# Kernel tuning notes

Hardware: AMD Instinct MI355X
Metric: run time of the kernel (lower is better)

## Reference

```python
import jax, jax.numpy as jnp
import numpy as np
import math

B, SV, ST, D, H = 16, 1024, 512, 768, 8
DH = D // H


def layernorm(x, g, b, eps=1e-5):
    m = jnp.mean(x, axis=-1, keepdims=True)
    v = jnp.var(x, axis=-1, keepdims=True)
    return (x - m) / jnp.sqrt(v + eps) * g + b


def setup_inputs() -> dict:
    key = jax.random.key(0)
    ks = jax.random.split(key, 12)
    s = 1.0 / math.sqrt(D)
    inp = {
        "visual_features": jax.random.normal(ks[0], (B, SV, D), jnp.float32),
        "text_features": jax.random.normal(ks[1], (B, ST, D), jnp.float32),
        "visual_mask": jnp.ones((B, SV), jnp.int32),
        "text_mask": jnp.ones((B, ST), jnp.int32),
        "Wq": jax.random.normal(ks[2], (D, D), jnp.float32) * s,
        "bq": jnp.zeros((D,), jnp.float32),
        "Wk": jax.random.normal(ks[3], (D, D), jnp.float32) * s,
        "bk": jnp.zeros((D,), jnp.float32),
        "Wv": jax.random.normal(ks[4], (D, D), jnp.float32) * s,
        "bv": jnp.zeros((D,), jnp.float32),
        "Wo": jax.random.normal(ks[5], (D, D), jnp.float32) * s,
        "bo": jnp.zeros((D,), jnp.float32),
        "ln1_g": jnp.ones((D,), jnp.float32),
        "ln1_b": jnp.zeros((D,), jnp.float32),
        "Wf": jax.random.normal(ks[6], (2 * D, D), jnp.float32) * (1.0 / math.sqrt(2 * D)),
        "bf": jnp.zeros((D,), jnp.float32),
        "ln2_g": jnp.ones((D,), jnp.float32),
        "ln2_b": jnp.zeros((D,), jnp.float32),
    }
    return inp


def _heads(x):
    b, s, _ = x.shape
    return x.reshape(b, s, H, DH)


def _cross_attn(q_feats, kv_feats, kv_mask, Wq, bq, Wk, bk, Wv, bv):
    # q_feats: [B,Sq,D], kv_feats: [B,Sk,D], kv_mask: [B,Sk] or None
    q = _heads(q_feats @ Wq + bq)   # [B,Sq,H,DH]
    k = _heads(kv_feats @ Wk + bk)  # [B,Sk,H,DH]
    v = _heads(kv_feats @ Wv + bv)
    scores = jnp.einsum('bqhd,bkhd->bhqk', q, k) / math.sqrt(DH)
    if kv_mask is not None:
        scores = jnp.where(kv_mask[:, None, None, :] == 0, -jnp.inf, scores)
    attn = jax.nn.softmax(scores, axis=-1)  # dropout is identity in eval
    out = jnp.einsum('bhqk,bkhd->bqhd', attn, v)
    return out.reshape(q_feats.shape[0], q_feats.shape[1], D)


def reference(visual_features, text_features, visual_mask, text_mask,
              Wq, bq, Wk, bk, Wv, bv, Wo, bo, ln1_g, ln1_b,
              Wf, bf, ln2_g, ln2_b):
    # visual queries attend to text
    v2t = _cross_attn(visual_features, text_features, text_mask, Wq, bq, Wk, bk, Wv, bv)
    # text queries attend to visual
    t2v = _cross_attn(text_features, visual_features, visual_mask, Wq, bq, Wk, bk, Wv, bv)
    attended_visual = layernorm(visual_features + (v2t @ Wo + bo), ln1_g, ln1_b)
    attended_text = layernorm(text_features + (t2v @ Wo + bo), ln1_g, ln1_b)
    # masked mean pooling
    vm = visual_mask[:, :, None].astype(jnp.float32)
    pooled_v = (attended_visual * vm).sum(1) / vm.sum(1)
    tm = text_mask[:, :, None].astype(jnp.float32)
    pooled_t = (attended_text * tm).sum(1) / tm.sum(1)
    fused = jnp.concatenate([pooled_v, pooled_t], axis=-1) @ Wf + bf
    fused = layernorm(fused, ln2_g, ln2_b)  # dropout identity in eval
    return fused
```

## Files before the change

kernel.cpp:

```cpp
#include <hip/hip_runtime.h>

typedef __bf16 bf16x8 __attribute__((ext_vector_type(8)));
typedef float f32x4 __attribute__((ext_vector_type(4)));
typedef unsigned short u16;
typedef unsigned int u32;
typedef u16 u16x8 __attribute__((ext_vector_type(8)));
typedef u16 u16x4 __attribute__((ext_vector_type(4)));


__device__ __forceinline__ u16 f2bf(float f) {
    u32 u = __builtin_bit_cast(u32, f);
    u32 r = u + 0x7FFFu + ((u >> 16) & 1u);
    return (u16)(r >> 16);
}

__device__ __forceinline__ float bf2f(u16 b) {
    u32 u = ((u32)b) << 16;
    return __builtin_bit_cast(float, u);
}

__device__ __forceinline__ f32x4 mfma16(bf16x8 a, bf16x8 b, f32x4 c) {
    return __builtin_amdgcn_mfma_f32_16x16x32_bf16(a, b, c, 0, 0, 0);
}

#define GLOAD_LDS16(g, l) __builtin_amdgcn_global_load_lds( \
    (__attribute__((address_space(1))) void*)(g), \
    (__attribute__((address_space(3))) void*)(l), 16, 0, 0)


__global__ __launch_bounds__(256) void k_cvt_x(const float* __restrict__ vf,
                                               const float* __restrict__ tf,
                                               u16* __restrict__ X, int nvis4) {
    int i = blockIdx.x * 256 + threadIdx.x;
    f32x4 v = (i < nvis4) ? ((const f32x4*)vf)[i] : ((const f32x4*)tf)[i - nvis4];
    u16x4 o = { f2bf(v[0]), f2bf(v[1]), f2bf(v[2]), f2bf(v[3]) };
    ((u16x4*)X)[i] = o;
}

__global__ __launch_bounds__(256) void k_transpose(const float* __restrict__ src,
                                                   u16* __restrict__ dst,
                                                   int K0, int N0) {
    __shared__ float t[64][65];
    int ntx = N0 >> 6;
    int k0 = (blockIdx.x / ntx) << 6, n0 = (blockIdx.x % ntx) << 6;
    int c = threadIdx.x & 63, rr = threadIdx.x >> 6;
#pragma unroll
    for (int q = 0; q < 16; q++) {
        int r = q * 4 + rr;
        t[r][c] = src[(size_t)(k0 + r) * N0 + n0 + c];
    }
    __syncthreads();
#pragma unroll
    for (int q = 0; q < 16; q++) {
        int r = q * 4 + rr;
        dst[(size_t)(n0 + r) * K0 + k0 + c] = f2bf(t[c][r]);
    }
}

__global__ __launch_bounds__(256) void k_bias(const float* __restrict__ bq,
                                              const float* __restrict__ bk,
                                              const float* __restrict__ bv,
                                              float* __restrict__ bqkv) {
    int n = blockIdx.x * 256 + threadIdx.x;
    if (n < 2304) {
        const float* s = (n < 768) ? bq : ((n < 1536) ? bk : bv);
        int r = (n < 768) ? n : ((n < 1536) ? n - 768 : n - 1536);
        bqkv[n] = s[r];
    }
}

__global__ __launch_bounds__(256) void k_zero(float* __restrict__ p) {
    p[blockIdx.x * 256 + threadIdx.x] = 0.f;
}

template <bool OUT_BF16, bool ADD_RES, bool SPLIT_VT>
__global__ __launch_bounds__(256) void k_gemm(const u16* __restrict__ A,
                                              const u16* __restrict__ Bt,
                                              const float* __restrict__ bias,
                                              const float* __restrict__ resA,
                                              const float* __restrict__ resB,
                                              void* __restrict__ Cout,
                                              int Ndim, int Kdim, int mvisL,
                                              u16* __restrict__ VtGp, int Rtot) {
    __shared__ alignas(16) u16 sA[2][128 * 32];
    __shared__ alignas(16) u16 sB[2][128 * 32];
    const int tid = threadIdx.x, wid = tid >> 6, lane = tid & 63;
    const int nwg = gridDim.x;
    const int wg = (blockIdx.x & 7) * (nwg >> 3) + (blockIdx.x >> 3);
    const int ntiles = Ndim >> 7;
    const int mt = wg / ntiles, nt = wg - mt * ntiles;
    const int m0 = mt << 7, n0 = nt << 7;
    const int wm = wid >> 1, wn = wid & 1;
    f32x4 acc[4][4] = {};

    const int r0 = tid >> 2, p0 = tid & 3;
    const int r1 = 64 + r0;
    const u16* ga0 = A + (size_t)(m0 + r0) * Kdim + p0 * 8;
    const u16* ga1 = A + (size_t)(m0 + r1) * Kdim + p0 * 8;
    const u16* gb0 = Bt + (size_t)(n0 + r0) * Kdim + p0 * 8;
    const u16* gb1 = Bt + (size_t)(n0 + r1) * Kdim + p0 * 8;
    const int loff0 = wid * 512;
    const int loff1 = 2048 + wid * 512;

    const int arow = (wm << 6) + (lane & 15);
    const int brow = (wn << 6) + (lane & 15);
    const int kg = (lane >> 4) * 8;

    auto stage = [&](int kt, int pb) {
        GLOAD_LDS16(ga0 + kt, &sA[pb][loff0]);
        GLOAD_LDS16(ga1 + kt, &sA[pb][loff1]);
        GLOAD_LDS16(gb0 + kt, &sB[pb][loff0]);
        GLOAD_LDS16(gb1 + kt, &sB[pb][loff1]);
    };

    const int niter = Kdim >> 5;
    stage(0, 0);
    for (int it = 0; it < niter; ++it) {
        const int cur = it & 1;
        __syncthreads();
        if (it + 1 < niter) stage((it + 1) << 5, cur ^ 1);
        bf16x8 av[4], bw[4];
#pragma unroll
        for (int i = 0; i < 4; i++) av[i] = *(const bf16x8*)&sA[cur][(arow + i * 16) * 32 + kg];
#pragma unroll
        for (int j = 0; j < 4; j++) bw[j] = *(const bf16x8*)&sB[cur][(brow + j * 16) * 32 + kg];
#pragma unroll
        for (int i = 0; i < 4; i++)
#pragma unroll
            for (int j = 0; j < 4; j++) acc[i][j] = mfma16(av[i], bw[j], acc[i][j]);
    }

    const int col0 = n0 + (wn << 6) + (lane & 15);
    const int rowb = m0 + (wm << 6) + ((lane >> 4) << 2);
    float bvals[4];
#pragma unroll
    for (int j = 0; j < 4; j++) bvals[j] = bias[col0 + j * 16];

    if constexpr (SPLIT_VT) {
        if (n0 >= 1536) {
            const int vcol0 = col0 - 1536;
#pragma unroll
            for (int i = 0; i < 4; i++) {
#pragma unroll
                for (int j = 0; j < 4; j++) {
                    u16x4 o4;
#pragma unroll
                    for (int rg = 0; rg < 4; rg++) o4[rg] = f2bf(acc[i][j][rg] + bvals[j]);
                    *(u16x4*)&VtGp[(size_t)(vcol0 + j * 16) * Rtot + rowb + i * 16] = o4;
                }
            }
            return;
        }
    }

#pragma unroll
    for (int i = 0; i < 4; i++) {
#pragma unroll
        for (int rg = 0; rg < 4; rg++) {
            const int row = rowb + i * 16 + rg;
            const float* rp = nullptr;
            if constexpr (ADD_RES)
                rp = (row < mvisL) ? resA + (size_t)row * 768
                                   : resB + (size_t)(row - mvisL) * 768;
#pragma unroll
            for (int j = 0; j < 4; j++) {
                const int col = col0 + j * 16;
                float v = acc[i][j][rg] + bvals[j];
                if constexpr (ADD_RES) v += rp[col];
                if constexpr (OUT_BF16)
                    ((u16*)Cout)[(size_t)row * Ndim + col] = f2bf(v);
                else
                    ((float*)Cout)[(size_t)row * Ndim + col] = v;
            }
        }
    }
}

__global__ __launch_bounds__(512) void k_attn(const u16* __restrict__ qkv,
                                              const u16* __restrict__ VtG,
                                              const int* __restrict__ vmaskc,
                                              const int* __restrict__ tmaskc,
                                              u16* __restrict__ attn, int CHn, int Rtot) {
    __shared__ alignas(16) u16 Kl[2][128 * 128];
    __shared__ alignas(16) u16 Vt[2][96 * 128];
    __shared__ alignas(16) u16 Pl[8][16 * 128];
    __shared__ float mk[2][128];

    const int bx = blockIdx.x;
    int b, h, qbase, kbase, nqt, ntl;
    const int* mask;
    const int vcap = CHn * 8;
    if (bx < vcap) {
        b = bx >> 3; h = bx & 7;
        qbase = b << 10; kbase = (CHn << 10) + (b << 9);
        mask = tmaskc + (b << 9); nqt = 4; ntl = 2;
    } else {
        const int bx2 = bx - vcap;
        b = bx2 >> 3; h = bx2 & 7;
        qbase = (CHn << 10) + (b << 9); kbase = b << 10;
        mask = vmaskc + (b << 10); nqt = 2; ntl = 3;
    }
    const int ntile = 1 << ntl;
    const int nsteps = nqt << ntl;
    const int tid = threadIdx.x, wid = tid >> 6, lane = tid & 63;
    const int l15 = lane & 15, l4 = lane >> 4;
    const float scale = 0.10206207261596577f;

    int koff[4];
#pragma unroll
    for (int kk = 0; kk < 4; kk++) koff[kk] = ((kk * 4 + l4) ^ (l15 & 7)) << 3;

    auto kt_of = [&](int s) {
        const int qt = s >> ntl, ktr = s & (ntile - 1);
        return (qt & 1) ? (ntile - 1 - ktr) : ktr;
    };
    auto stage = [&](int kt, int pb) {
#pragma unroll
        for (int it = 0; it < 4; ++it) {
            const int cb = it * 512 + (wid << 6);
            const int c = cb + lane;
            const int r = c >> 4, s8 = c & 15;
            const int k8 = s8 ^ (r & 7);
            const u16* src = qkv + (size_t)(kbase + (kt << 7) + r) * 2304 + 768 + h * 96
                             + (k8 < 12 ? k8 * 8 : 0);
            GLOAD_LDS16(src, &Kl[pb][(size_t)cb * 8]);
        }
#pragma unroll
        for (int it = 0; it < 3; ++it) {
            const int cb = it * 512 + (wid << 6);
            const int c = cb + lane;
            const int d = c >> 4, s8 = c & 15;
            const int k8 = s8 ^ (d & 7);
            const u16* src = VtG + (size_t)(h * 96 + d) * Rtot + kbase + (kt << 7) + k8 * 8;
            GLOAD_LDS16(src, &Vt[pb][(size_t)cb * 8]);
        }
        if (tid < 128) mk[pb][tid] = mask[(kt << 7) + tid] ? 0.f : -1e30f;
    };

    stage(kt_of(0), 0);
    int s = 0;
    for (int qt = 0; qt < nqt; ++qt) {
        bf16x8 aq[2][3];
#pragma unroll
        for (int qs = 0; qs < 2; ++qs) {
            const int qr = qbase + (qt << 8) + (wid << 5) + qs * 16 + l15;
#pragma unroll
            for (int kk = 0; kk < 3; kk++) {
                bf16x8 tq = *(const bf16x8*)&qkv[(size_t)qr * 2304 + h * 96 + kk * 32 + l4 * 8];
#pragma unroll
                for (int e = 0; e < 8; e++) tq[e] = (__bf16)((float)tq[e] * scale);
                aq[qs][kk] = tq;
            }
        }
        f32x4 o[2][6] = {};
        float mrun[2][4], lrun[2][4];
#pragma unroll
        for (int qs = 0; qs < 2; ++qs)
#pragma unroll
            for (int rg = 0; rg < 4; rg++) { mrun[qs][rg] = -1e30f; lrun[qs][rg] = 0.f; }

        for (int ktr = 0; ktr < ntile; ++ktr, ++s) {
            const int cur = s & 1;
            __syncthreads();
            if (s + 1 < nsteps) stage(kt_of(s + 1), cur ^ 1);

            f32x4 sc[2][8];
#pragma unroll
            for (int j = 0; j < 8; j++) {
                const int rbase = (j * 16 + l15) * 128;
                bf16x8 bk[3];
#pragma unroll
                for (int kk = 0; kk < 3; kk++)
                    bk[kk] = *(const bf16x8*)&Kl[cur][rbase + koff[kk]];
#pragma unroll
                for (int qs = 0; qs < 2; ++qs) {
                    f32x4 cj = {0.f, 0.f, 0.f, 0.f};
#pragma unroll
                    for (int kk = 0; kk < 3; kk++) cj = mfma16(aq[qs][kk], bk[kk], cj);
                    sc[qs][j] = cj;
                }
            }

#pragma unroll
            for (int qs = 0; qs < 2; ++qs) {
                float tmax[4] = {-1e30f, -1e30f, -1e30f, -1e30f};
#pragma unroll
                for (int j = 0; j < 8; j++) {
                    float mb = mk[cur][j * 16 + l15];
#pragma unroll
                    for (int rg = 0; rg < 4; rg++) {
                        float v = sc[qs][j][rg] + mb;
                        sc[qs][j][rg] = v;
                        tmax[rg] = fmaxf(tmax[rg], v);
                    }
                }
#pragma unroll
                for (int d = 1; d < 16; d <<= 1)
#pragma unroll
                    for (int rg = 0; rg < 4; rg++)
                        tmax[rg] = fmaxf(tmax[rg], __shfl_xor(tmax[rg], d));
                int need = 0;
#pragma unroll
                for (int rg = 0; rg < 4; rg++) need |= (tmax[rg] > mrun[qs][rg] + 8.f) ? 1 : 0;
                if (__any(need)) {
#pragma unroll
                    for (int rg = 0; rg < 4; rg++) {
                        float mn = fmaxf(mrun[qs][rg], tmax[rg]);
                        float corr = __expf(mrun[qs][rg] - mn);
                        mrun[qs][rg] = mn;
                        lrun[qs][rg] *= corr;
#pragma unroll
                        for (int j6 = 0; j6 < 6; j6++) o[qs][j6][rg] *= corr;
                    }
                }
                float tsum[4] = {0.f, 0.f, 0.f, 0.f};
#pragma unroll
                for (int j = 0; j < 8; j++)
#pragma unroll
                    for (int rg = 0; rg < 4; rg++) {
                        float p = __expf(sc[qs][j][rg] - mrun[qs][rg]);
                        tsum[rg] += p;
                        const int prow = l4 * 4 + rg;
                        Pl[wid][prow * 128 + ((j * 16 + l15) ^ ((prow & 7) << 3))] = f2bf(p);
                    }
#pragma unroll
                for (int d = 1; d < 16; d <<= 1)
#pragma unroll
                    for (int rg = 0; rg < 4; rg++) tsum[rg] += __shfl_xor(tsum[rg], d);
#pragma unroll
                for (int rg = 0; rg < 4; rg++) lrun[qs][rg] += tsum[rg];

#pragma unroll
                for (int kk = 0; kk < 4; kk++) {
                    bf16x8 ap = *(const bf16x8*)&Pl[wid][l15 * 128 + koff[kk]];
#pragma unroll
                    for (int j6 = 0; j6 < 6; j6++) {
                        bf16x8 bv8 = *(const bf16x8*)&Vt[cur][(j6 * 16 + l15) * 128 + koff[kk]];
                        o[qs][j6] = mfma16(ap, bv8, o[qs][j6]);
                    }
                }
            }
        }

#pragma unroll
        for (int qs = 0; qs < 2; ++qs) {
            float inv[4];
#pragma unroll
            for (int rg = 0; rg < 4; rg++) inv[rg] = 1.f / lrun[qs][rg];
            const size_t orow = (size_t)(qbase + (qt << 8) + (wid << 5) + qs * 16);
#pragma unroll
            for (int j6 = 0; j6 < 6; j6++)
#pragma unroll
                for (int rg = 0; rg < 4; rg++)
                    attn[(orow + l4 * 4 + rg) * 768 + h * 96 + j6 * 16 + l15] =
                        f2bf(o[qs][j6][rg] * inv[rg]);
        }
    }
}

__global__ __launch_bounds__(256) void k_ln_pool(const u16* __restrict__ X,
                                                 const int* __restrict__ vmaskc,
                                                 const int* __restrict__ tmaskc,
                                                 const float* __restrict__ g,
                                                 const float* __restrict__ bb,
                                                 float* __restrict__ pooled,
                                                 int mvisL, int bg0) {
    __shared__ float pool[768];
    const int tid = threadIdx.x, wid = tid >> 6, lane = tid & 63;
    const int row0 = blockIdx.x << 5;
    const bool vis = row0 < mvisL;
    const int* mask = vis ? vmaskc : tmaskc;
    const int mbase = vis ? 0 : mvisL;
    const int bl = vis ? (row0 >> 10) : ((row0 - mvisL) >> 9);
    float* pout = pooled + (vis ? 0 : 12288) + (size_t)(bg0 + bl) * 768;

    float gv[12], bv2[12];
#pragma unroll
    for (int k = 0; k < 12; k++) { gv[k] = g[lane + k * 64]; bv2[k] = bb[lane + k * 64]; }
    float acc[12] = {};
    for (int rr = 0; rr < 8; ++rr) {
        const int row = row0 + (wid << 3) + rr;
        const u16* x = X + (size_t)row * 768;
        float xs[12], sm = 0.f, s2 = 0.f;
#pragma unroll
        for (int k = 0; k < 12; k++) {
            float tv = bf2f(x[lane + k * 64]);
            xs[k] = tv; sm += tv; s2 += tv * tv;
        }
#pragma unroll
        for (int d = 1; d < 64; d <<= 1) { sm += __shfl_xor(sm, d); s2 += __shfl_xor(s2, d); }
        const float mean = sm * (1.f / 768.f);
        const float rstd = rsqrtf(s2 * (1.f / 768.f) - mean * mean + 1e-5f);
        const float mv = (float)mask[row - mbase];
#pragma unroll
        for (int k = 0; k < 12; k++) acc[k] += ((xs[k] - mean) * rstd * gv[k] + bv2[k]) * mv;
    }
    pool[tid] = 0.f; pool[tid + 256] = 0.f; pool[tid + 512] = 0.f;
    __syncthreads();
#pragma unroll
    for (int k = 0; k < 12; k++) atomicAdd(&pool[lane + k * 64], acc[k]);
    __syncthreads();
    atomicAdd(&pout[tid], pool[tid]);
    atomicAdd(&pout[tid + 256], pool[tid + 256]);
    atomicAdd(&pout[tid + 512], pool[tid + 512]);
}

__device__ __forceinline__ float blk_sum(float v, volatile float* tmp) {
#pragma unroll
    for (int d = 1; d < 64; d <<= 1) v += __shfl_xor(v, d);
    __syncthreads();
    if ((threadIdx.x & 63) == 0) tmp[threadIdx.x >> 6] = v;
    __syncthreads();
    return tmp[0] + tmp[1] + tmp[2] + tmp[3];
}

__global__ __launch_bounds__(256) void k_final(const float* __restrict__ pooled,
                                               const int* __restrict__ vmask,
                                               const int* __restrict__ tmask,
                                               const float* __restrict__ Wf,
                                               const float* __restrict__ bfv,
                                               const float* __restrict__ g2,
                                               const float* __restrict__ b2,
                                               float* __restrict__ out) {
    __shared__ float sh[1536];
    __shared__ float red[4];
    const int b = blockIdx.x, tid = threadIdx.x;
    float cv = 0.f, ct = 0.f;
    for (int i = tid; i < 1024; i += 256) cv += (float)vmask[(b << 10) + i];
    for (int i = tid; i < 512; i += 256) ct += (float)tmask[(b << 9) + i];
    cv = blk_sum(cv, red);
    ct = blk_sum(ct, red);
    const float iv = 1.f / cv, itv = 1.f / ct;
#pragma unroll
    for (int k = 0; k < 3; k++) {
        int j = tid + (k << 8);
        sh[j] = pooled[b * 768 + j] * iv;
        sh[768 + j] = pooled[12288 + b * 768 + j] * itv;
    }
    __syncthreads();
    float f0 = bfv[tid], f1 = bfv[tid + 256], f2 = bfv[tid + 512];
    for (int i = 0; i < 1536; i++) {
        const float pv = sh[i];
        const float* w = Wf + (size_t)i * 768;
        f0 += pv * w[tid];
        f1 += pv * w[tid + 256];
        f2 += pv * w[tid + 512];
    }
    float sm = blk_sum(f0 + f1 + f2, red);
    float s2 = blk_sum(f0 * f0 + f1 * f1 + f2 * f2, red);
    const float mean = sm * (1.f / 768.f);
    const float rstd = rsqrtf(s2 * (1.f / 768.f) - mean * mean + 1e-5f);
    out[b * 768 + tid] = (f0 - mean) * rstd * g2[tid] + b2[tid];
    out[b * 768 + tid + 256] = (f1 - mean) * rstd * g2[tid + 256] + b2[tid + 256];
    out[b * 768 + tid + 512] = (f2 - mean) * rstd * g2[tid + 512] + b2[tid + 512];
}

extern "C" void kernel_launch(void* const* d_in, const int* in_sizes, int n_in,
                              void* d_out, int out_size, void* d_ws, size_t ws_size,
                              hipStream_t stream) {
    (void)in_sizes; (void)n_in; (void)out_size;
    const float* vf = (const float*)d_in[0];
    const float* tf = (const float*)d_in[1];
    const int* vmask = (const int*)d_in[2];
    const int* tmask = (const int*)d_in[3];
    const float* Wq = (const float*)d_in[4];
    const float* bq = (const float*)d_in[5];
    const float* Wk = (const float*)d_in[6];
    const float* bk = (const float*)d_in[7];
    const float* Wv = (const float*)d_in[8];
    const float* bv = (const float*)d_in[9];
    const float* Wo = (const float*)d_in[10];
    const float* bo = (const float*)d_in[11];
    const float* g1 = (const float*)d_in[12];
    const float* b1 = (const float*)d_in[13];
    const float* Wf = (const float*)d_in[14];
    const float* bfv = (const float*)d_in[15];
    const float* g2 = (const float*)d_in[16];
    const float* b2 = (const float*)d_in[17];
    float* outp = (float*)d_out;

    int CH = 16;
    while (CH > 1 && 4826112ull + (size_t)CH * 11796480ull > ws_size) CH >>= 1;
    const int NC = 16 / CH;
    const int Rtot = CH * 1536;

    char* ws = (char*)d_ws;
    u16*   wsW      = (u16*)(ws);
    u16*   wsWo     = (u16*)(ws + 3538944);
    float* wsBqkv   = (float*)(ws + 4718592);
    float* wsPooled = (float*)(ws + 4727808);
    u16*   wsX      = (u16*)(ws + 4826112);
    char*  qkvBase  = ws + 4826112 + (size_t)CH * 2359296;
    u16*   wsQKV    = (u16*)qkvBase;
    u16*   wsOproj  = (u16*)qkvBase;
    u16*   wsVtG    = (u16*)(qkvBase + (size_t)CH * 7077888);
    u16*   wsAttn   = wsX;

    k_transpose<<<dim3(144), dim3(256), 0, stream>>>(Wq, wsW, 768, 768);
    k_transpose<<<dim3(144), dim3(256), 0, stream>>>(Wk, wsW + 589824, 768, 768);
    k_transpose<<<dim3(144), dim3(256), 0, stream>>>(Wv, wsW + 1179648, 768, 768);
    k_transpose<<<dim3(144), dim3(256), 0, stream>>>(Wo, wsWo, 768, 768);
    k_bias<<<dim3(9), dim3(256), 0, stream>>>(bq, bk, bv, wsBqkv);
    k_zero<<<dim3(96), dim3(256), 0, stream>>>(wsPooled);

    for (int c = 0; c < NC; ++c) {
        const float* vfc = vf + (size_t)c * CH * 1024 * 768;
        const float* tfc = tf + (size_t)c * CH * 512 * 768;
        const int* vmc = vmask + c * CH * 1024;
        const int* tmc = tmask + c * CH * 512;

        k_cvt_x<<<dim3(CH * 1152), dim3(256), 0, stream>>>(vfc, tfc, wsX, CH * 196608);

        k_gemm<true, false, true><<<dim3(CH * 216), dim3(256), 0, stream>>>(
            wsX, wsW, wsBqkv, nullptr, nullptr, (void*)wsQKV, 2304, 768, 0, wsVtG, Rtot);

        k_attn<<<dim3(CH * 16), dim3(512), 0, stream>>>(
            wsQKV, wsVtG, vmc, tmc, wsAttn, CH, Rtot);

        k_gemm<true, true, false><<<dim3(CH * 72), dim3(256), 0, stream>>>(
            wsAttn, wsWo, bo, vfc, tfc, (void*)wsOproj, 768, 768, CH * 1024, nullptr, 0);

        k_ln_pool<<<dim3(CH * 48), dim3(256), 0, stream>>>(
            wsOproj, vmc, tmc, g1, b1, wsPooled, CH * 1024, c * CH);
    }

    k_final<<<dim3(16), dim3(256), 0, stream>>>(wsPooled, vmask, tmask, Wf, bfv, g2, b2, outp);
}
```

Measured before the change: 457.1 us.

## Keep softmax probabilities in registers via transposed QK^T and 16x16x16 PV MFMA

Swaps the operands of the QK^T MFMA so each lane holds scores for one query row across four key positions. That output layout then feeds directly as the A operand of a 16x16x16 bf16 MFMA for P·V, which removes the per-warp LDS round trip for P. Row max and sum reductions shrink from 4-step shuffles over 16 lanes to two cross-group shuffles with per-row scalars, and the correction factors are broadcast back with shuffles. In exchange it issues twice as many smaller-K MFMAs for P·V and reads V as 8-byte fragments.

Result: faster. 433.9 us (-5.1%).

```diff
diff --git a/kernel.cpp b/kernel.cpp
--- a/kernel.cpp
+++ b/kernel.cpp
@@ -1,6 +1,8 @@
 #include <hip/hip_runtime.h>
 
 typedef __bf16 bf16x8 __attribute__((ext_vector_type(8)));
+typedef __bf16 bf16x4v __attribute__((ext_vector_type(4)));
+typedef short s16x4 __attribute__((ext_vector_type(4)));
 typedef float f32x4 __attribute__((ext_vector_type(4)));
 typedef unsigned short u16;
 typedef unsigned int u32;
@@ -21,6 +23,20 @@
 
 __device__ __forceinline__ f32x4 mfma16(bf16x8 a, bf16x8 b, f32x4 c) {
     return __builtin_amdgcn_mfma_f32_16x16x32_bf16(a, b, c, 0, 0, 0);
+}
+
+__device__ __forceinline__ f32x4 mfma16k16(bf16x4v a, bf16x4v b, f32x4 c) {
+#if __has_builtin(__builtin_amdgcn_mfma_f32_16x16x16_bf16)
+    return __builtin_amdgcn_mfma_f32_16x16x16_bf16(a, b, c, 0, 0, 0);
+#elif __has_builtin(__builtin_amdgcn_mfma_f32_16x16x16bf16_1k)
+    return __builtin_amdgcn_mfma_f32_16x16x16bf16_1k(
+        __builtin_bit_cast(s16x4, a), __builtin_bit_cast(s16x4, b), c, 0, 0, 0);
+#else
+    f32x4 d;
+    asm volatile("v_mfma_f32_16x16x16_bf16 %0, %1, %2, %3"
+                 : "=v"(d) : "v"(a), "v"(b), "v"(c));
+    return d;
+#endif
 }
 
 #define GLOAD_LDS16(g, l) __builtin_amdgcn_global_load_lds( \
@@ -183,7 +199,6 @@
                                               u16* __restrict__ attn, int CHn, int Rtot) {
     __shared__ alignas(16) u16 Kl[2][128 * 128];
     __shared__ alignas(16) u16 Vt[2][96 * 128];
-    __shared__ alignas(16) u16 Pl[8][16 * 128];
     __shared__ float mk[2][128];
 
     const int bx = blockIdx.x;
@@ -206,9 +221,9 @@
     const int l15 = lane & 15, l4 = lane >> 4;
     const float scale = 0.10206207261596577f;
 
-    int koff[4];
-#pragma unroll
-    for (int kk = 0; kk < 4; kk++) koff[kk] = ((kk * 4 + l4) ^ (l15 & 7)) << 3;
+    int koff[3];
+#pragma unroll
+    for (int kk = 0; kk < 3; kk++) koff[kk] = ((kk * 4 + l4) ^ (l15 & 7)) << 3;
 
     auto kt_of = [&](int s) {
         const int qt = s >> ntl, ktr = s & (ntile - 1);
@@ -253,11 +268,8 @@
             }
         }
         f32x4 o[2][6] = {};
-        float mrun[2][4], lrun[2][4];
-#pragma unroll
-        for (int qs = 0; qs < 2; ++qs)
-#pragma unroll
-            for (int rg = 0; rg < 4; rg++) { mrun[qs][rg] = -1e30f; lrun[qs][rg] = 0.f; }
+        float mrunS[2] = {-1e30f, -1e30f};
+        float lrunS[2] = {0.f, 0.f};
 
         for (int ktr = 0; ktr < ntile; ++ktr, ++s) {
             const int cur = s & 1;
@@ -276,77 +288,79 @@
                 for (int qs = 0; qs < 2; ++qs) {
                     f32x4 cj = {0.f, 0.f, 0.f, 0.f};
 #pragma unroll
-                    for (int kk = 0; kk < 3; kk++) cj = mfma16(aq[qs][kk], bk[kk], cj);
+                    for (int kk = 0; kk < 3; kk++) cj = mfma16(bk[kk], aq[qs][kk], cj);
                     sc[qs][j] = cj;
                 }
             }
 
+            bf16x4v pb[2][8];
 #pragma unroll
             for (int qs = 0; qs < 2; ++qs) {
-                float tmax[4] = {-1e30f, -1e30f, -1e30f, -1e30f};
+                float tm = -1e30f;
 #pragma unroll
                 for (int j = 0; j < 8; j++) {
-                    float mb = mk[cur][j * 16 + l15];
+                    f32x4 m4 = *(const f32x4*)&mk[cur][j * 16 + (l4 << 2)];
 #pragma unroll
                     for (int rg = 0; rg < 4; rg++) {
-                        float v = sc[qs][j][rg] + mb;
+                        float v = sc[qs][j][rg] + m4[rg];
                         sc[qs][j][rg] = v;
-                        tmax[rg] = fmaxf(tmax[rg], v);
+                        tm = fmaxf(tm, v);
                     }
                 }
-#pragma unroll
-                for (int d = 1; d < 16; d <<= 1)
-#pragma unroll
-                    for (int rg = 0; rg < 4; rg++)
-                        tmax[rg] = fmaxf(tmax[rg], __shfl_xor(tmax[rg], d));
-                int need = 0;
-#pragma unroll
-                for (int rg = 0; rg < 4; rg++) need |= (tmax[rg] > mrun[qs][rg] + 8.f) ? 1 : 0;
+                tm = fmaxf(tm, __shfl_xor(tm, 16));
+                tm = fmaxf(tm, __shfl_xor(tm, 32));
+                const int need = (tm > mrunS[qs] + 8.f) ? 1 : 0;
                 if (__any(need)) {
+                    float mn = fmaxf(mrunS[qs], tm);
+                    float corrS = __expf(mrunS[qs] - mn);
+                    mrunS[qs] = mn;
+                    lrunS[qs] *= corrS;
+                    float cr[4];
+#pragma unroll
+                    for (int rg = 0; rg < 4; rg++) cr[rg] = __shfl(corrS, (l4 << 2) + rg);
+#pragma unroll
+                    for (int j6 = 0; j6 < 6; j6++)
+#pragma unroll
+                        for (int rg = 0; rg < 4; rg++) o[qs][j6][rg] *= cr[rg];
+                }
+                float ts = 0.f;
+#pragma unroll
+                for (int j = 0; j < 8; j++) {
+                    bf16x4v pq;
 #pragma unroll
                     for (int rg = 0; rg < 4; rg++) {
-                        float mn = fmaxf(mrun[qs][rg], tmax[rg]);
-                        float corr = __expf(mrun[qs][rg] - mn);
-                        mrun[qs][rg] = mn;
-                        lrun[qs][rg] *= corr;
-#pragma unroll
-                        for (int j6 = 0; j6 < 6; j6++) o[qs][j6][rg] *= corr;
+                        float p = __expf(sc[qs][j][rg] - mrunS[qs]);
+                        ts += p;
+                        pq[rg] = (__bf16)p;
                     }
+                    pb[qs][j] = pq;
                 }
-                float tsum[4] = {0.f, 0.f, 0.f, 0.f};
-#pragma unroll
-                for (int j = 0; j < 8; j++)
-#pragma unroll
-                    for (int rg = 0; rg < 4; rg++) {
-                        float p = __expf(sc[qs][j][rg] - mrun[qs][rg]);
-                        tsum[rg] += p;
-                        const int prow = l4 * 4 + rg;
-                        Pl[wid][prow * 128 + ((j * 16 + l15) ^ ((prow & 7) << 3))] = f2bf(p);
-                    }
-#pragma unroll
-                for (int d = 1; d < 16; d <<= 1)
-#pragma unroll
-                    for (int rg = 0; rg < 4; rg++) tsum[rg] += __shfl_xor(tsum[rg], d);
-#pragma unroll
-                for (int rg = 0; rg < 4; rg++) lrun[qs][rg] += tsum[rg];
-
-#pragma unroll
-                for (int kk = 0; kk < 4; kk++) {
-                    bf16x8 ap = *(const bf16x8*)&Pl[wid][l15 * 128 + koff[kk]];
-#pragma unroll
-                    for (int j6 = 0; j6 < 6; j6++) {
-                        bf16x8 bv8 = *(const bf16x8*)&Vt[cur][(j6 * 16 + l15) * 128 + koff[kk]];
-                        o[qs][j6] = mfma16(ap, bv8, o[qs][j6]);
-                    }
+                ts += __shfl_xor(ts, 16);
+                ts += __shfl_xor(ts, 32);
+                lrunS[qs] += ts;
+            }
+
+#pragma unroll
+            for (int j = 0; j < 8; j++) {
+                const int slotb = 2 * j + (l4 >> 1);
+                const int intra = (l4 & 1) << 2;
+#pragma unroll
+                for (int j6 = 0; j6 < 6; j6++) {
+                    const int d = j6 * 16 + l15;
+                    bf16x4v bv = *(const bf16x4v*)&Vt[cur][d * 128 +
+                                     ((slotb ^ (l15 & 7)) << 3) + intra];
+                    o[0][j6] = mfma16k16(pb[0][j], bv, o[0][j6]);
+                    o[1][j6] = mfma16k16(pb[1][j], bv, o[1][j6]);
                 }
             }
         }
 
 #pragma unroll
         for (int qs = 0; qs < 2; ++qs) {
+            const float invS = 1.f / lrunS[qs];
             float inv[4];
 #pragma unroll
-            for (int rg = 0; rg < 4; rg++) inv[rg] = 1.f / lrun[qs][rg];
+            for (int rg = 0; rg < 4; rg++) inv[rg] = __shfl(invS, (l4 << 2) + rg);
             const size_t orow = (size_t)(qbase + (qt << 8) + (wid << 5) + qs * 16);
 #pragma unroll
             for (int j6 = 0; j6 < 6; j6++)
```
